# Kernel optimization log

Hardware: AMD Instinct MI355X
Metric: run time of the kernel (lower is better)

Reference implementation:

```python
import jax, jax.numpy as jnp
import numpy as np

GRID_N = 3   # number of grid intervals (pykan 'grid')
K = 3        # spline order (pykan 'k')
IN_F = 512
OUT_F = 512
BATCH = 8
SEQ = 2048


def _extended_grid(d, dtype):
    # base grid: num+1 points over [-1, 1]; extend by K steps of h on each side (pykan extend_grid)
    pts = jnp.linspace(-1.0, 1.0, GRID_N + 1).astype(dtype)
    h = jnp.asarray(2.0 / GRID_N, dtype)
    left = pts[0] + h * jnp.arange(-K, 0, dtype=dtype)
    right = pts[-1] + h * jnp.arange(1, K + 1, dtype=dtype)
    ext = jnp.concatenate([left, pts, right])           # (GRID_N + 1 + 2K,)
    return jnp.broadcast_to(ext, (d, ext.shape[0]))     # per-input-feature grid (shared values)


def _bspline_basis(x, grid):
    # Cox-de Boor recursion, vectorized over tokens and input features.
    # x: (N, D), grid: (D, M) -> returns (N, D, M-1-K) = (N, D, GRID_N+K)
    x = x[:, :, None]                     # (N, D, 1)
    g = grid[None, :, :]                  # (1, D, M)
    B = ((x >= g[..., :-1]) & (x < g[..., 1:])).astype(x.dtype)
    for p in range(1, K + 1):
        left = (x - g[..., :-(p + 1)]) / (g[..., p:-1] - g[..., :-(p + 1)])
        right = (g[..., p + 1:] - x) / (g[..., p + 1:] - g[..., 1:-p])
        B = left * B[..., :-1] + right * B[..., 1:]
    return B


def setup_inputs() -> dict:
    key = jax.random.key(0)
    k1, k2, k3 = jax.random.split(key, 3)
    x = jax.random.normal(k1, (BATCH, SEQ, IN_F), dtype=jnp.float32)
    coef = jax.random.normal(k2, (OUT_F, IN_F, GRID_N + K), dtype=jnp.float32) * 0.1
    scale_base = (1.0 / np.sqrt(IN_F)) + (jax.random.uniform(k3, (OUT_F, IN_F), dtype=jnp.float32) * 2.0 - 1.0) * 0.1
    scale_sp = jnp.ones((OUT_F, IN_F), dtype=jnp.float32)
    bias = jnp.zeros((OUT_F,), dtype=jnp.float32)
    return {"x": x, "coef": coef, "scale_base": scale_base, "scale_sp": scale_sp, "bias": bias}


def reference(x, coef, scale_base, scale_sp, bias):
    B_, S, D = x.shape
    xf = x.reshape(-1, D)                               # (N, D) tokens
    grid = _extended_grid(D, xf.dtype)
    basis = _bspline_basis(xf, grid)                    # (N, D, GRID_N+K)
    base = jax.nn.silu(xf)                              # base activation per input feature
    # per-edge: scale_base*silu(x_i) + scale_sp*spline(x_i); sum over input features, add bias
    spline_w = scale_sp[..., None] * coef               # (O, D, GRID_N+K)
    y = (jnp.einsum('ni,oi->no', base, scale_base)
         + jnp.einsum('nib,oib->no', basis, spline_w)
         + bias[None, :])
    return y.reshape(B_, S, -1)
```

## Files before the change

### kernel.cpp

```cpp
#include <hip/hip_runtime.h>


typedef short        bf16x8 __attribute__((ext_vector_type(8)));
typedef float        f32x4  __attribute__((ext_vector_type(4)));
typedef unsigned int u32x4  __attribute__((ext_vector_type(4)));

#define NROWS 16384
#define DIN   512
#define DOUT  512
#define BM    64
#define BN    256
#define NKT   64

__device__ __forceinline__ unsigned short f2bf(float f) {
    unsigned int u = __float_as_uint(f);
    u += 0x7fffu + ((u >> 16) & 1u);
    return (unsigned short)(u >> 16);
}

__device__ __forceinline__ void kan_act_store(float xv, char* p16) {
    float S  = __builtin_fmaf(xv, 1.5f, 4.5f);
    float jf = floorf(S);
    float t  = S - jf;
    int   j  = (int)jf;
    float t2 = t * t;
    float t3 = t2 * t;
    float omt  = 1.0f - t;
    float omt2 = omt * omt;
    float n0 = omt2 * omt * (1.0f / 6.0f);
    float n1 = __builtin_fmaf(t3, 0.5f, -t2) + (2.0f / 3.0f);
    float u  = (t + t2) - t3;
    float n2 = __builtin_fmaf(u, 0.5f, 1.0f / 6.0f);
    float n3 = t3 * (1.0f / 6.0f);
    float e  = __expf(-xv);
    float si = xv * __builtin_amdgcn_rcpf(1.0f + e);

    unsigned P01, P23, WS;
    asm("v_cvt_pk_bf16_f32 %0, %1, %2" : "=v"(P01) : "v"(n0), "v"(n1));
    asm("v_cvt_pk_bf16_f32 %0, %1, %2" : "=v"(P23) : "v"(n2), "v"(n3));
    asm("v_cvt_pk_bf16_f32 %0, %1, %2" : "=v"(WS)  : "v"(si), "v"(0.0f));
    unsigned U = P01 << 16;
    unsigned V = (P01 >> 16) | (P23 << 16);
    unsigned Z = P23 >> 16;
    bool odd = (j & 1) != 0;
    unsigned c0 = odd ? U : P01;
    unsigned c1 = odd ? V : P23;
    unsigned c2 = odd ? Z : 0u;
    int b = (j - 2) >> 1;
    u32x4 w;
    w[0] = (b == 0) ? c0 : (b == -1) ? c1 : (b == -2) ? c2 : 0u;
    w[1] = (b == 1) ? c0 : (b ==  0) ? c1 : (b == -1) ? c2 : 0u;
    w[2] = (b == 2) ? c0 : (b ==  1) ? c1 : (b ==  0) ? c2 : 0u;
    w[3] = (b == 3) ? c0 : (b ==  2) ? c1 : (b ==  1) ? c2 : 0u;
    w[0] = (w[0] & 0xFFFF0000u) | (WS & 0xFFFFu);
    *(u32x4*)p16 = w;
}

__global__ __launch_bounds__(256) void kan_prep(
    const float* __restrict__ coef, const float* __restrict__ scale_base,
    const float* __restrict__ scale_sp, unsigned short* __restrict__ wt)
{
    int t = blockIdx.x * 256 + threadIdx.x;
    int o = t >> 9;
    int i = t & 511;
    float sb = scale_base[t];
    float sp = scale_sp[t];
    const float* cp = coef + (size_t)t * 6;
    bf16x8 w;
    w[0] = (short)f2bf(sb);
#pragma unroll
    for (int b = 0; b < 6; ++b) w[1 + b] = (short)f2bf(sp * cp[b]);
    w[7] = 0;
    int nt = o >> 8, ol = o & 255;
    int kt = i >> 3, s = i & 7, ks = s >> 2, fg = s & 3;
    size_t off = (size_t)nt * 2097152
               + (size_t)((kt * 2 + ks) * 256 + ol) * 64 + fg * 16;
    *(bf16x8*)((char*)wt + off) = w;
}

__global__ __launch_bounds__(256, 2) void kan_gemm(
    const float* __restrict__ x, const unsigned short* __restrict__ wt,
    const float* __restrict__ bias, float* __restrict__ y)
{
    __shared__ char As[2][BM * 128];

    const int tid  = threadIdx.x;
    const int lane = tid & 63;
    const int wid  = tid >> 6;

    int bid = blockIdx.x;
    int wg  = (bid & 7) * 64 + (bid >> 3);
    int mt  = wg & 255;
    int nt  = wg >> 8;

    const int row0 = mt * BM;
    const int col0 = nt * BN;

    const int ar = tid >> 2;
    const int ap = tid & 3;
    const float* xp = x + (size_t)(row0 + ar) * DIN + ap * 2;
    const int as_sw = (ar & 7) << 4;
    const int c0 = (ap * 2) << 4;

    const int fr = lane & 15;
    const int fg = lane >> 4;

    const char* wb = (const char*)wt + (size_t)nt * 2097152;
    int colpart[4];
#pragma unroll
    for (int n2 = 0; n2 < 4; ++n2)
        colpart[n2] = (wid * 64 + n2 * 16 + fr) * 64 + fg * 16;

#define LOADB(B, ktv)                                                         \
    {                                                                         \
        _Pragma("unroll")                                                     \
        for (int q = 0; q < 8; ++q) {                                         \
            int n2_ = q & 3, ks_ = q >> 2;                                    \
            B[q] = *(const bf16x8*)(wb + (size_t)((ktv) * 2 + ks_) * 16384    \
                                    + colpart[n2_]);                          \
        }                                                                     \
    }

    f32x4 acc[4][4];
#pragma unroll
    for (int m2 = 0; m2 < 4; ++m2)
#pragma unroll
        for (int n2 = 0; n2 < 4; ++n2) {
            f32x4 z = {0.f, 0.f, 0.f, 0.f};
            acc[m2][n2] = z;
        }

    bf16x8 Ba[8], Bb[8];

    LOADB(Ba, 0);
    {
        float2 xa = *(const float2*)(xp);
        char* rowp = &As[0][ar * 128];
        kan_act_store(xa.x, rowp + (c0 ^ as_sw));
        kan_act_store(xa.y, rowp + ((c0 + 16) ^ as_sw));
    }
    float2 xb = *(const float2*)(xp + 8);
    asm volatile("s_waitcnt lgkmcnt(0)" ::: "memory");
    __builtin_amdgcn_s_barrier();

#define STEP(ktv, Bcur, Bnext)                                                \
    {                                                                         \
        const int cur_ = (ktv) & 1, nxt_ = cur_ ^ 1;                          \
        bf16x8 af_[2][4];                                                     \
        _Pragma("unroll")                                                     \
        for (int ks_ = 0; ks_ < 2; ++ks_) {                                   \
            _Pragma("unroll")                                                 \
            for (int m2_ = 0; m2_ < 4; ++m2_) {                               \
                int rr_ = m2_ * 16 + fr;                                      \
                af_[ks_][m2_] = *(const bf16x8*)(&As[cur_][0] + rr_ * 128     \
                    + ((ks_ * 64 + fg * 16) ^ ((rr_ & 7) << 4)));             \
            }                                                                 \
        }                                                                     \
        if ((ktv) + 1 < NKT) {                                                \
            LOADB(Bnext, (ktv) + 1);                                          \
            char* rowp_ = &As[nxt_][ar * 128];                                \
            kan_act_store(xb.x, rowp_ + (c0 ^ as_sw));                        \
            kan_act_store(xb.y, rowp_ + ((c0 + 16) ^ as_sw));                 \
            if ((ktv) + 2 < NKT)                                              \
                xb = *(const float2*)(xp + ((ktv) + 2) * 8);                  \
        }                                                                     \
        __builtin_amdgcn_s_setprio(1);                                        \
        _Pragma("unroll")                                                     \
        for (int ks_ = 0; ks_ < 2; ++ks_)                                     \
            _Pragma("unroll")                                                 \
            for (int m2_ = 0; m2_ < 4; ++m2_)                                 \
                _Pragma("unroll")                                             \
                for (int n2_ = 0; n2_ < 4; ++n2_)                             \
                    acc[m2_][n2_] = __builtin_amdgcn_mfma_f32_16x16x32_bf16(  \
                        af_[ks_][m2_], Bcur[ks_ * 4 + n2_], acc[m2_][n2_],    \
                        0, 0, 0);                                             \
        __builtin_amdgcn_s_setprio(0);                                        \
        asm volatile("s_waitcnt lgkmcnt(0)" ::: "memory");                    \
        __builtin_amdgcn_s_barrier();                                         \
    }

    for (int kt = 0; kt < NKT; kt += 2) {
        STEP(kt, Ba, Bb);
        STEP(kt + 1, Bb, Ba);
    }

    const int orow0 = row0 + fg * 4;
    const int ocol0 = col0 + wid * 64 + fr;
#pragma unroll
    for (int n2 = 0; n2 < 4; ++n2) {
        float bv = bias[ocol0 + n2 * 16];
#pragma unroll
        for (int m2 = 0; m2 < 4; ++m2) {
#pragma unroll
            for (int r = 0; r < 4; ++r) {
                y[(size_t)(orow0 + m2 * 16 + r) * DOUT + (ocol0 + n2 * 16)]
                    = acc[m2][n2][r] + bv;
            }
        }
    }
#undef STEP
#undef LOADB
}

extern "C" void kernel_launch(void* const* d_in, const int* in_sizes, int n_in,
                              void* d_out, int out_size, void* d_ws, size_t ws_size,
                              hipStream_t stream)
{
    const float* x          = (const float*)d_in[0];
    const float* coef       = (const float*)d_in[1];
    const float* scale_base = (const float*)d_in[2];
    const float* scale_sp   = (const float*)d_in[3];
    const float* bias       = (const float*)d_in[4];
    unsigned short* wt = (unsigned short*)d_ws;
    float* y = (float*)d_out;

    kan_prep<<<1024, 256, 0, stream>>>(coef, scale_base, scale_sp, wt);
    kan_gemm<<<512, 256, 0, stream>>>(x, wt, bias, y);
}
```

Before: 81.73 us.

## Widen GEMM tile to full output width so activations compute once per row

Changes the block tile from 64x256 to 64x512 with 8 waves per block, so each token row's B-spline/SiLU activation expansion is computed only once instead of once per N tile. The weight layout in the prep kernel drops the N-tile split to match, and the grid halves to 256 blocks. The trade-off is fewer blocks (256 on a device with many CUs, so less than one block per CU pair) and more register and launch-bound pressure per block.

```diff
diff --git a/kernel.cpp b/kernel.cpp
--- a/kernel.cpp
+++ b/kernel.cpp
@@ -9,7 +9,7 @@
 #define DIN   512
 #define DOUT  512
 #define BM    64
-#define BN    256
+#define BN    512
 #define NKT   64
 
 __device__ __forceinline__ unsigned short f2bf(float f) {
@@ -71,14 +71,12 @@
 #pragma unroll
     for (int b = 0; b < 6; ++b) w[1 + b] = (short)f2bf(sp * cp[b]);
     w[7] = 0;
-    int nt = o >> 8, ol = o & 255;
     int kt = i >> 3, s = i & 7, ks = s >> 2, fg = s & 3;
-    size_t off = (size_t)nt * 2097152
-               + (size_t)((kt * 2 + ks) * 256 + ol) * 64 + fg * 16;
+    size_t off = ((size_t)((kt * 2 + ks) * 512 + o)) * 64 + fg * 16;
     *(bf16x8*)((char*)wt + off) = w;
 }
 
-__global__ __launch_bounds__(256, 2) void kan_gemm(
+__global__ __launch_bounds__(512, 2) void kan_gemm(
     const float* __restrict__ x, const unsigned short* __restrict__ wt,
     const float* __restrict__ bias, float* __restrict__ y)
 {
@@ -89,23 +87,22 @@
     const int wid  = tid >> 6;
 
     int bid = blockIdx.x;
-    int wg  = (bid & 7) * 64 + (bid >> 3);
-    int mt  = wg & 255;
-    int nt  = wg >> 8;
+    int mt  = (bid & 7) * 32 + (bid >> 3);
 
     const int row0 = mt * BM;
-    const int col0 = nt * BN;
-
-    const int ar = tid >> 2;
-    const int ap = tid & 3;
-    const float* xp = x + (size_t)(row0 + ar) * DIN + ap * 2;
+
+    const int ar = tid >> 3;
+    const int ap = tid & 7;
+    const float* xp = x + (size_t)(row0 + ar) * DIN + ap;
     const int as_sw = (ar & 7) << 4;
-    const int c0 = (ap * 2) << 4;
+    const int c0 = ap << 4;
+    char* const arow0 = &As[0][ar * 128];
+    char* const arow1 = &As[1][ar * 128];
 
     const int fr = lane & 15;
     const int fg = lane >> 4;
 
-    const char* wb = (const char*)wt + (size_t)nt * 2097152;
+    const char* wb = (const char*)wt;
     int colpart[4];
 #pragma unroll
     for (int n2 = 0; n2 < 4; ++n2)
@@ -116,7 +113,7 @@
         _Pragma("unroll")                                                     \
         for (int q = 0; q < 8; ++q) {                                         \
             int n2_ = q & 3, ks_ = q >> 2;                                    \
-            B[q] = *(const bf16x8*)(wb + (size_t)((ktv) * 2 + ks_) * 16384    \
+            B[q] = *(const bf16x8*)(wb + (size_t)((ktv) * 2 + ks_) * 32768    \
                                     + colpart[n2_]);                          \
         }                                                                     \
     }
@@ -133,19 +130,14 @@
     bf16x8 Ba[8], Bb[8];
 
     LOADB(Ba, 0);
-    {
-        float2 xa = *(const float2*)(xp);
-        char* rowp = &As[0][ar * 128];
-        kan_act_store(xa.x, rowp + (c0 ^ as_sw));
-        kan_act_store(xa.y, rowp + ((c0 + 16) ^ as_sw));
-    }
-    float2 xb = *(const float2*)(xp + 8);
+    kan_act_store(xp[0], arow0 + (c0 ^ as_sw));
+    float xb = xp[8];
     asm volatile("s_waitcnt lgkmcnt(0)" ::: "memory");
     __builtin_amdgcn_s_barrier();
 
 #define STEP(ktv, Bcur, Bnext)                                                \
     {                                                                         \
-        const int cur_ = (ktv) & 1, nxt_ = cur_ ^ 1;                          \
+        const int cur_ = (ktv) & 1;                                           \
         bf16x8 af_[2][4];                                                     \
         _Pragma("unroll")                                                     \
         for (int ks_ = 0; ks_ < 2; ++ks_) {                                   \
@@ -158,11 +150,9 @@
         }                                                                     \
         if ((ktv) + 1 < NKT) {                                                \
             LOADB(Bnext, (ktv) + 1);                                          \
-            char* rowp_ = &As[nxt_][ar * 128];                                \
-            kan_act_store(xb.x, rowp_ + (c0 ^ as_sw));                        \
-            kan_act_store(xb.y, rowp_ + ((c0 + 16) ^ as_sw));                 \
-            if ((ktv) + 2 < NKT)                                              \
-                xb = *(const float2*)(xp + ((ktv) + 2) * 8);                  \
+            char* rowp_ = (((ktv) + 1) & 1) ? arow1 : arow0;                  \
+            kan_act_store(xb, rowp_ + (c0 ^ as_sw));                          \
+            if ((ktv) + 2 < NKT) xb = xp[((ktv) + 2) * 8];                    \
         }                                                                     \
         __builtin_amdgcn_s_setprio(1);                                        \
         _Pragma("unroll")                                                     \
@@ -185,7 +175,7 @@
     }
 
     const int orow0 = row0 + fg * 4;
-    const int ocol0 = col0 + wid * 64 + fr;
+    const int ocol0 = wid * 64 + fr;
 #pragma unroll
     for (int n2 = 0; n2 < 4; ++n2) {
         float bv = bias[ocol0 + n2 * 16];
@@ -215,5 +205,5 @@
     float* y = (float*)d_out;
 
     kan_prep<<<1024, 256, 0, stream>>>(coef, scale_base, scale_sp, wt);
-    kan_gemm<<<512, 256, 0, stream>>>(x, wt, bias, y);
-}
+    kan_gemm<<<256, 512, 0, stream>>>(x, wt, bias, y);
+}
```

Result: slower. 91.01 us (+11.4%).

## Batch four K-steps per LDS stage to cut barriers per iteration

Applied to the files above, without the earlier changes.

The A-tile LDS buffer grows from one K-step per stage to four, so workgroup barriers and lgkmcnt waits happen once per four K-steps instead of every step. Four x prefetch registers are kept live so the activation for the next stage can be computed while the current one is consumed. The cost is 4x the LDS footprint (64KB total) and more live registers, which may reduce occupancy at the two-blocks-per-CU launch bound.

```diff
diff --git a/kernel.cpp b/kernel.cpp
--- a/kernel.cpp
+++ b/kernel.cpp
@@ -11,6 +11,7 @@
 #define BM    64
 #define BN    256
 #define NKT   64
+#define NSS   16
 
 __device__ __forceinline__ unsigned short f2bf(float f) {
     unsigned int u = __float_as_uint(f);
@@ -82,7 +83,7 @@
     const float* __restrict__ x, const unsigned short* __restrict__ wt,
     const float* __restrict__ bias, float* __restrict__ y)
 {
-    __shared__ char As[2][BM * 128];
+    __shared__ char As[2][4][BM * 128];
 
     const int tid  = threadIdx.x;
     const int lane = tid & 63;
@@ -133,36 +134,41 @@
     bf16x8 Ba[8], Bb[8];
 
     LOADB(Ba, 0);
-    {
-        float2 xa = *(const float2*)(xp);
-        char* rowp = &As[0][ar * 128];
+#pragma unroll
+    for (int j = 0; j < 4; ++j) {
+        float2 xa = *(const float2*)(xp + j * 8);
+        char* rowp = &As[0][j][ar * 128];
         kan_act_store(xa.x, rowp + (c0 ^ as_sw));
         kan_act_store(xa.y, rowp + ((c0 + 16) ^ as_sw));
     }
-    float2 xb = *(const float2*)(xp + 8);
+    float2 xq0 = *(const float2*)(xp + 4 * 8);
+    float2 xq1 = *(const float2*)(xp + 5 * 8);
+    float2 xq2 = *(const float2*)(xp + 6 * 8);
+    float2 xq3 = *(const float2*)(xp + 7 * 8);
     asm volatile("s_waitcnt lgkmcnt(0)" ::: "memory");
     __builtin_amdgcn_s_barrier();
 
-#define STEP(ktv, Bcur, Bnext)                                                \
+#define SUBSTEP(jc, Bcur, Bnext, xq)                                          \
     {                                                                         \
-        const int cur_ = (ktv) & 1, nxt_ = cur_ ^ 1;                          \
+        const int kt_ = ss * 4 + (jc);                                        \
+        const int cur_ = ss & 1;                                              \
         bf16x8 af_[2][4];                                                     \
         _Pragma("unroll")                                                     \
         for (int ks_ = 0; ks_ < 2; ++ks_) {                                   \
             _Pragma("unroll")                                                 \
             for (int m2_ = 0; m2_ < 4; ++m2_) {                               \
                 int rr_ = m2_ * 16 + fr;                                      \
-                af_[ks_][m2_] = *(const bf16x8*)(&As[cur_][0] + rr_ * 128     \
+                af_[ks_][m2_] = *(const bf16x8*)(&As[cur_][jc][0] + rr_ * 128 \
                     + ((ks_ * 64 + fg * 16) ^ ((rr_ & 7) << 4)));             \
             }                                                                 \
         }                                                                     \
-        if ((ktv) + 1 < NKT) {                                                \
-            LOADB(Bnext, (ktv) + 1);                                          \
-            char* rowp_ = &As[nxt_][ar * 128];                                \
-            kan_act_store(xb.x, rowp_ + (c0 ^ as_sw));                        \
-            kan_act_store(xb.y, rowp_ + ((c0 + 16) ^ as_sw));                 \
-            if ((ktv) + 2 < NKT)                                              \
-                xb = *(const float2*)(xp + ((ktv) + 2) * 8);                  \
+        if (kt_ + 1 < NKT) LOADB(Bnext, kt_ + 1);                             \
+        if (ss + 1 < NSS) {                                                   \
+            char* rowp_ = &As[cur_ ^ 1][jc][ar * 128];                        \
+            kan_act_store(xq.x, rowp_ + (c0 ^ as_sw));                        \
+            kan_act_store(xq.y, rowp_ + ((c0 + 16) ^ as_sw));                 \
+            if (ss + 2 < NSS)                                                 \
+                xq = *(const float2*)(xp + ((ss + 2) * 4 + (jc)) * 8);        \
         }                                                                     \
         __builtin_amdgcn_s_setprio(1);                                        \
         _Pragma("unroll")                                                     \
@@ -175,13 +181,15 @@
                         af_[ks_][m2_], Bcur[ks_ * 4 + n2_], acc[m2_][n2_],    \
                         0, 0, 0);                                             \
         __builtin_amdgcn_s_setprio(0);                                        \
-        asm volatile("s_waitcnt lgkmcnt(0)" ::: "memory");                    \
-        __builtin_amdgcn_s_barrier();                                         \
-    }
-
-    for (int kt = 0; kt < NKT; kt += 2) {
-        STEP(kt, Ba, Bb);
-        STEP(kt + 1, Bb, Ba);
+    }
+
+    for (int ss = 0; ss < NSS; ++ss) {
+        SUBSTEP(0, Ba, Bb, xq0);
+        SUBSTEP(1, Bb, Ba, xq1);
+        SUBSTEP(2, Ba, Bb, xq2);
+        SUBSTEP(3, Bb, Ba, xq3);
+        asm volatile("s_waitcnt lgkmcnt(0)" ::: "memory");
+        __builtin_amdgcn_s_barrier();
     }
 
     const int orow0 = row0 + fg * 4;
@@ -198,7 +206,7 @@
             }
         }
     }
-#undef STEP
+#undef SUBSTEP
 #undef LOADB
 }
 
```

After: 81.36 us. No clear change (-0.4%).
